# Kernel tuning notes

Hardware: AMD Instinct MI355X
Metric: run time of the kernel (lower is better)

The kernel has to match this reference:

```python
import jax, jax.numpy as jnp
import numpy as np

EMB = 1024
NH = 16
HS = EMB // NH

def setup_inputs() -> dict:
    key = jax.random.key(0)
    ks = jax.random.split(key, 9)
    s = 0.02
    x = jax.random.normal(ks[0], (4, 2048, EMB), dtype=jnp.float32)
    Wq = jax.random.normal(ks[1], (EMB, EMB), dtype=jnp.float32) * s
    bq = jnp.zeros((EMB,), jnp.float32)
    Wk = jax.random.normal(ks[2], (EMB, EMB), dtype=jnp.float32) * s
    bk = jnp.zeros((EMB,), jnp.float32)
    Wv = jax.random.normal(ks[3], (EMB, EMB), dtype=jnp.float32) * s
    bv = jnp.zeros((EMB,), jnp.float32)
    Wo = jax.random.normal(ks[4], (EMB, EMB), dtype=jnp.float32) * s
    bo = jnp.zeros((EMB,), jnp.float32)
    return {"x": x, "Wq": Wq, "bq": bq, "Wk": Wk, "bk": bk,
            "Wv": Wv, "bv": bv, "Wo": Wo, "bo": bo}

def reference(x, Wq, bq, Wk, bk, Wv, bv, Wo, bo):
    B, T, C = x.shape
    q = x @ Wq + bq
    k = x @ Wk + bk
    v = x @ Wv + bv
    # [B, H, T, hs]
    q = q.reshape(B, T, NH, HS).transpose(0, 2, 1, 3)
    k = k.reshape(B, T, NH, HS).transpose(0, 2, 1, 3)
    v = v.reshape(B, T, NH, HS).transpose(0, 2, 1, 3)
    scale = 1.0 / np.sqrt(HS).astype(np.float32)
    att = jnp.einsum('bhqd,bhkd->bhqk', q, k) * scale
    causal = jnp.tril(jnp.ones((T, T), dtype=bool))
    att = jnp.where(causal[None, None], att, jnp.float32(-jnp.inf))
    att = jax.nn.softmax(att, axis=-1)
    y = jnp.einsum('bhqk,bhkd->bhqd', att, v)
    y = y.transpose(0, 2, 1, 3).reshape(B, T, C)
    return y @ Wo + bo
```

## Files before the change

kernel.cpp:

```cpp
#include <hip/hip_runtime.h>

#define EMB   1024
#define NHEAD 16
#define HS    64
#define BATCH 4
#define SEQ   2048
#define MTOK  (BATCH*SEQ)

typedef __bf16 bf16;
typedef __bf16 bf16x8 __attribute__((ext_vector_type(8)));
typedef __bf16 bf16x4 __attribute__((ext_vector_type(4)));
typedef float  f32x4  __attribute__((ext_vector_type(4)));
typedef _Float16 f16;
typedef f16 f16x4 __attribute__((ext_vector_type(4)));
typedef f16 f16x8 __attribute__((ext_vector_type(8)));

#define MFMA16(a,b,c)     __builtin_amdgcn_mfma_f32_16x16x32_bf16(a,b,c,0,0,0)
#define MFMA_H32(a,b,c)   __builtin_amdgcn_mfma_f32_16x16x32_f16(a,b,c,0,0,0)
#define MFMA_H16(a,b,c)   __builtin_amdgcn_mfma_f32_16x16x16f16(a,b,c,0,0,0)

#if __has_builtin(__builtin_amdgcn_exp2f)
#define EXP2(x) __builtin_amdgcn_exp2f(x)
#else
#define EXP2(x) exp2f(x)
#endif

#define GLL(g, l) __builtin_amdgcn_global_load_lds(                         \
        (const __attribute__((address_space(1))) void*)(g),                 \
        (__attribute__((address_space(3))) void*)(l), 16, 0, 0)

__global__ __launch_bounds__(256) void k_prep(
        const float* __restrict__ x, bf16* __restrict__ xb,
        const float* __restrict__ W0, const float* __restrict__ W1,
        const float* __restrict__ W2, const float* __restrict__ W3,
        bf16* __restrict__ T0, bf16* __restrict__ T1,
        bf16* __restrict__ T2, bf16* __restrict__ T3) {
    const int z = blockIdx.z;
    if (z == 0) {
        const int blk = blockIdx.y * 16 + blockIdx.x;
        const size_t base = (size_t)blk * 32768;
        for (int j = threadIdx.x; j < 8192; j += 256) {
            size_t i = base + (size_t)j * 4;
            float4 v = *(const float4*)(x + i);
            bf16x4 o;
            o[0] = (bf16)v.x; o[1] = (bf16)v.y; o[2] = (bf16)v.z; o[3] = (bf16)v.w;
            *(bf16x4*)(xb + i) = o;
        }
        return;
    }
    __shared__ float tile[64][65];
    const float* W = (z == 1) ? W0 : (z == 2) ? W1 : (z == 3) ? W2 : W3;
    bf16* Wt = (z == 1) ? T0 : (z == 2) ? T1 : (z == 3) ? T2 : T3;
    int c0 = blockIdx.x * 64, r0 = blockIdx.y * 64;
    int tx = threadIdx.x & 63, ty = threadIdx.x >> 6;
    #pragma unroll
    for (int r = ty; r < 64; r += 4)
        tile[r][tx] = W[(r0 + r) * EMB + c0 + tx];
    __syncthreads();
    #pragma unroll
    for (int cc = ty; cc < 64; cc += 4)
        Wt[(c0 + cc) * EMB + r0 + tx] = (bf16)tile[tx][cc];
}

__global__ __launch_bounds__(512, 2) void k_qkv_gemm(
        const bf16* __restrict__ xb,
        const bf16* __restrict__ Wqt, const bf16* __restrict__ Wkt, const bf16* __restrict__ Wvt,
        const float* __restrict__ bq, const float* __restrict__ bk, const float* __restrict__ bv,
        f16* __restrict__ Q, f16* __restrict__ K, f16* __restrict__ Vt) {
    __shared__ __align__(16) bf16 As[2][8192];
    __shared__ __align__(16) bf16 Bs[2][8192];
    const int tid = threadIdx.x;
    const int lane = tid & 63;
    const int l15 = lane & 15, quad = lane >> 4;
    const int wave = tid >> 6;
    const int wm = wave >> 2;
    const int wn = wave & 3;

    const int mt = blockIdx.x;
    const int nt = blockIdx.y;
    const int which = nt >> 2;
    const int n0 = (nt & 3) * 256;

    const bf16* Wt   = (which == 0) ? Wqt : (which == 1) ? Wkt : Wvt;
    const float* bias = (which == 0) ? bq : (which == 1) ? bk : bv;

    const bf16* Abase = xb + (size_t)mt * 256 * EMB;
    const bf16* Bbase = Wt + (size_t)n0 * EMB;

    const int P   = tid >> 3, s8 = tid & 7;
    const int cch = s8 ^ (P & 7);
    const int r_  = 2 * P + (cch >> 2);
    const int kc8 = (cch & 3) * 8;
    const bf16* Asrc = Abase + (size_t)r_ * EMB + kc8;
    const bf16* Bsrc = Bbase + (size_t)r_ * EMB + kc8;

#define STAGE_A(T, cb) do {                                                  \
    GLL(Asrc + (T) * 32,             &As[cb][tid * 8]);                      \
    GLL(Asrc + 128 * EMB + (T) * 32, &As[cb][tid * 8 + 4096]); } while (0)
#define STAGE_B(T, cb) do {                                                  \
    GLL(Bsrc + (T) * 32,             &Bs[cb][tid * 8]);                      \
    GLL(Bsrc + 128 * EMB + (T) * 32, &Bs[cb][tid * 8 + 4096]); } while (0)

    int aoff[8], boff[4];
    #pragma unroll
    for (int mf = 0; mf < 8; mf++) {
        const int row = wm * 128 + mf * 16 + l15;
        const int Pr = row >> 1, hh = row & 1;
        aoff[mf] = Pr * 64 + ((((hh << 2) | quad)) ^ (Pr & 7)) * 8;
    }
    #pragma unroll
    for (int nf = 0; nf < 4; nf++) {
        const int row = wn * 64 + nf * 16 + l15;
        const int Pr = row >> 1, hh = row & 1;
        boff[nf] = Pr * 64 + ((((hh << 2) | quad)) ^ (Pr & 7)) * 8;
    }

    f32x4 acc[8][4];
    #pragma unroll
    for (int i = 0; i < 8; i++)
        #pragma unroll
        for (int j = 0; j < 4; j++) acc[i][j] = (f32x4){0.f, 0.f, 0.f, 0.f};

#define BARX __builtin_amdgcn_s_barrier()
#define PRI1 __builtin_amdgcn_s_setprio(1)
#define PRI0 __builtin_amdgcn_s_setprio(0)
#define SCHB __builtin_amdgcn_sched_barrier(0)
#define VM0 asm volatile("s_waitcnt vmcnt(0)" ::: "memory")

    STAGE_A(0, 0); STAGE_B(0, 0);
    SCHB; VM0; BARX;

    bf16x8 a[4], b[4], a2[4];
    #pragma unroll 1
    for (int W = 0; W < 31; ++W) {
        const int c = W & 1;
        const bf16* Ab = As[c];
        const bf16* Bb = Bs[c];
        #pragma unroll
        for (int i = 0; i < 4; i++) a[i] = *(const bf16x8*)(Ab + aoff[i]);
        #pragma unroll
        for (int j = 0; j < 4; j++) b[j] = *(const bf16x8*)(Bb + boff[j]);
        STAGE_A(W + 1, c ^ 1);
        SCHB;
        BARX; PRI1;
        #pragma unroll
        for (int i = 0; i < 4; i++)
            #pragma unroll
            for (int j = 0; j < 4; j++)
                acc[i][j] = MFMA16(a[i], b[j], acc[i][j]);
        PRI0;
        #pragma unroll
        for (int i = 0; i < 4; i++) a2[i] = *(const bf16x8*)(Ab + aoff[4 + i]);
        STAGE_B(W + 1, c ^ 1);
        SCHB; VM0; BARX;
        PRI1;
        #pragma unroll
        for (int i = 0; i < 4; i++)
            #pragma unroll
            for (int j = 0; j < 4; j++)
                acc[4 + i][j] = MFMA16(a2[i], b[j], acc[4 + i][j]);
        PRI0;
    }
    {
        const bf16* Ab = As[1];
        const bf16* Bb = Bs[1];
        #pragma unroll
        for (int i = 0; i < 4; i++) a[i] = *(const bf16x8*)(Ab + aoff[i]);
        #pragma unroll
        for (int j = 0; j < 4; j++) b[j] = *(const bf16x8*)(Bb + boff[j]);
        #pragma unroll
        for (int i = 0; i < 4; i++) a2[i] = *(const bf16x8*)(Ab + aoff[4 + i]);
        #pragma unroll
        for (int i = 0; i < 4; i++)
            #pragma unroll
            for (int j = 0; j < 4; j++) {
                acc[i][j]     = MFMA16(a[i],  b[j], acc[i][j]);
                acc[4 + i][j] = MFMA16(a2[i], b[j], acc[4 + i][j]);
            }
    }
#undef STAGE_A
#undef STAGE_B

    const float QSCALE = 0.18033688011112043f;
    const int h = (n0 >> 6) + wn;
    if (which == 2) {
        #pragma unroll
        for (int nf = 0; nf < 4; nf++) {
            const float bv_ = bias[n0 + wn * 64 + nf * 16 + l15];
            const int d = nf * 16 + l15;
            #pragma unroll
            for (int mf = 0; mf < 8; mf++) {
                const int row0 = mt * 256 + wm * 128 + mf * 16 + quad * 4;
                const int b_ = row0 >> 11, tk0 = row0 & (SEQ - 1);
                f16x4 vv;
                #pragma unroll
                for (int r = 0; r < 4; r++) vv[r] = (f16)(acc[mf][nf][r] + bv_);
                *(f16x4*)(Vt + (((size_t)(b_ * NHEAD + h) * 32 + (tk0 >> 6)) * 64 + d) * 64
                          + (tk0 & 63)) = vv;
            }
        }
    } else {
        f16* OUT = (which == 0) ? Q : K;
        const float scl = (which == 0) ? QSCALE : 1.0f;
        float bvv[4];
        #pragma unroll
        for (int nf = 0; nf < 4; nf++) bvv[nf] = bias[n0 + wn * 64 + nf * 16 + l15];
        #pragma unroll
        for (int mf = 0; mf < 8; mf++) {
            const int row0 = mt * 256 + wm * 128 + mf * 16 + quad * 4;
            const int b_ = row0 >> 11, tk0 = row0 & (SEQ - 1);
            #pragma unroll
            for (int r = 0; r < 4; r++) {
                f16* op = OUT + ((size_t)(b_ * NHEAD + h) * SEQ + (tk0 + r)) * HS + l15;
                #pragma unroll
                for (int nf = 0; nf < 4; nf++)
                    op[nf * 16] = (f16)((acc[mf][nf][r] + bvv[nf]) * scl);
            }
        }
    }
}

__global__ __launch_bounds__(256) void k_attn(
        const f16* __restrict__ Q, const f16* __restrict__ K,
        const f16* __restrict__ Vt, bf16* __restrict__ y) {
    __shared__ __align__(16) f16 kbuf[2][64 * 64];
    __shared__ __align__(16) f16 vbuf[2][64 * 64];
    const int tid = threadIdx.x;
    const int wave = tid >> 6, lane = tid & 63;
    const int l15 = lane & 15, quad = lane >> 4;

    const int L = blockIdx.x;
    const int xcd = L & 7, s = L >> 3;
    const int bh = xcd * 8 + (s & 7);
    const int qt = 15 - (s >> 3);
    const int h = bh & (NHEAD - 1), b_ = bh >> 4;

    const f16* Qb = Q + (size_t)bh * SEQ * HS;
    const f16* Kb = K + (size_t)bh * SEQ * HS;
    const f16* Vb = Vt + (size_t)bh * 32 * 4096;

    const int c0 = tid, c1 = tid + 256;
    const int soff0 = (c0 >> 3) * 64 + (((c0 & 7) ^ ((c0 >> 3) & 7)) * 8);
    const int soff1 = (c1 >> 3) * 64 + (((c1 & 7) ^ ((c1 >> 3) & 7)) * 8);
    const int swz = l15 & 7;

    f16x4 ones;
    #pragma unroll
    for (int i = 0; i < 4; i++) ones[i] = (f16)1.0f;

    const int ntiles = 2 * qt + 2;
    const int qrow0 = qt * 128 + wave * 32;

    f16x8 qb[2][2];
    #pragma unroll
    for (int qf = 0; qf < 2; qf++)
        #pragma unroll
        for (int dk = 0; dk < 2; dk++)
            qb[qf][dk] = *(const f16x8*)(Qb + (qrow0 + 16 * qf + l15) * HS + 32 * dk + quad * 8);

    f32x4 o[2][4], lacc[2];
    #pragma unroll
    for (int qf = 0; qf < 2; qf++) {
        lacc[qf] = (f32x4){0.f, 0.f, 0.f, 0.f};
        #pragma unroll
        for (int df = 0; df < 4; df++) o[qf][df] = (f32x4){0.f, 0.f, 0.f, 0.f};
    }

    f16x8 kr0 = *(const f16x8*)(Kb + c0 * 8);
    f16x8 kr1 = *(const f16x8*)(Kb + c1 * 8);
    f16x8 vr0 = *(const f16x8*)(Vb + c0 * 8);
    f16x8 vr1 = *(const f16x8*)(Vb + c1 * 8);
    *(f16x8*)(kbuf[0] + soff0) = kr0;
    *(f16x8*)(kbuf[0] + soff1) = kr1;
    *(f16x8*)(vbuf[0] + soff0) = vr0;
    *(f16x8*)(vbuf[0] + soff1) = vr1;

    for (int it = 0; it < ntiles; ++it) {
        const int kv0 = it * 64;
        __syncthreads();
        if (it + 1 < ntiles) {
            const f16* kg = Kb + (size_t)(kv0 + 64) * HS;
            const f16* vg = Vb + (size_t)(it + 1) * 4096;
            kr0 = *(const f16x8*)(kg + c0 * 8);
            kr1 = *(const f16x8*)(kg + c1 * 8);
            vr0 = *(const f16x8*)(vg + c0 * 8);
            vr1 = *(const f16x8*)(vg + c1 * 8);
        }
        if (kv0 <= qrow0 + 31) {
            const f16* kb_ = kbuf[it & 1];
            const f16* vb_ = vbuf[it & 1];

            f32x4 sreg[4][2];
            #pragma unroll
            for (int mb = 0; mb < 4; mb++) {
                f16x8 ka0 = *(const f16x8*)(kb_ + (16 * mb + l15) * 64 + ((quad ^ swz) * 8));
                f16x8 ka1 = *(const f16x8*)(kb_ + (16 * mb + l15) * 64 + (((4 + quad) ^ swz) * 8));
                #pragma unroll
                for (int qf = 0; qf < 2; qf++) {
                    f32x4 t = (f32x4){0.f, 0.f, 0.f, 0.f};
                    t = MFMA_H32(ka0, qb[qf][0], t);
                    t = MFMA_H32(ka1, qb[qf][1], t);
                    sreg[mb][qf] = t;
                }
            }

            f16x4 pa[4][2];
            const bool edge = (kv0 + 63 > qrow0);
            #pragma unroll
            for (int mb = 0; mb < 4; mb++)
                #pragma unroll
                for (int qf = 0; qf < 2; qf++) {
                    f16x4 p;
                    if (edge) {
                        #pragma unroll
                        for (int r = 0; r < 4; r++) {
                            const int kvc = kv0 + 16 * mb + quad * 4 + r;
                            const int qq  = qrow0 + 16 * qf + l15;
                            p[r] = (f16)((kvc <= qq) ? EXP2(sreg[mb][qf][r]) : 0.f);
                        }
                    } else {
                        #pragma unroll
                        for (int r = 0; r < 4; r++)
                            p[r] = (f16)EXP2(sreg[mb][qf][r]);
                    }
                    pa[mb][qf] = p;
                }

            #pragma unroll
            for (int df = 0; df < 4; df++)
                #pragma unroll
                for (int kb = 0; kb < 4; kb++) {
                    f16x4 vfrag = *(const f16x4*)(vb_ + (16 * df + l15) * 64 +
                                    (((2 * kb + (quad >> 1)) ^ swz) * 8) + (quad & 1) * 4);
                    #pragma unroll
                    for (int qf = 0; qf < 2; qf++)
                        o[qf][df] = MFMA_H16(pa[kb][qf], vfrag, o[qf][df]);
                }
            #pragma unroll
            for (int kb = 0; kb < 4; kb++)
                #pragma unroll
                for (int qf = 0; qf < 2; qf++)
                    lacc[qf] = MFMA_H16(pa[kb][qf], ones, lacc[qf]);
        }
        if (it + 1 < ntiles) {
            const int nb = (it + 1) & 1;
            *(f16x8*)(kbuf[nb] + soff0) = kr0;
            *(f16x8*)(kbuf[nb] + soff1) = kr1;
            *(f16x8*)(vbuf[nb] + soff0) = vr0;
            *(f16x8*)(vbuf[nb] + soff1) = vr1;
        }
    }

    #pragma unroll
    for (int qf = 0; qf < 2; qf++)
        #pragma unroll
        for (int r = 0; r < 4; r++) {
            float inv = 1.f / lacc[qf][r];
            int t = qrow0 + 16 * qf + quad * 4 + r;
            bf16* yp = y + ((size_t)(b_ * SEQ + t)) * EMB + h * HS;
            #pragma unroll
            for (int df = 0; df < 4; df++)
                yp[df * 16 + l15] = (bf16)(o[qf][df][r] * inv);
        }
}

__global__ __launch_bounds__(256) void k_out_gemm(
        const bf16* __restrict__ y, const bf16* __restrict__ Wot,
        const float* __restrict__ bo, float* __restrict__ out) {
    __shared__ __align__(16) bf16 As[128 * 64];
    __shared__ __align__(16) bf16 Bs[128 * 64];
    const int tid = threadIdx.x;
    const int lane = tid & 63;
    const int wave = tid >> 6;
    const int l15 = lane & 15, quad = lane >> 4;
    const int wm = (wave >> 1) * 64, wn = (wave & 1) * 64;
    const int m0 = blockIdx.x * 128;
    const int n0 = blockIdx.y * 128;

    f32x4 acc[4][4];
    #pragma unroll
    for (int i = 0; i < 4; i++)
        #pragma unroll
        for (int j = 0; j < 4; j++) acc[i][j] = (f32x4){0.f, 0.f, 0.f, 0.f};

    const int r0_ = tid >> 3;
    const int kcs = ((tid & 7) ^ (r0_ & 7)) * 8;
    const bf16* Ag = y   + (size_t)m0 * EMB + r0_ * EMB + kcs;
    const bf16* Bg = Wot + (size_t)n0 * EMB + r0_ * EMB + kcs;
    const int rsw = l15 & 7;

    for (int k0 = 0; k0 < EMB; k0 += 64) {
        __syncthreads();
        #pragma unroll
        for (int g = 0; g < 4; g++) {
            GLL(Ag + 32 * g * EMB + k0, As + (tid + g * 256) * 8);
            GLL(Bg + 32 * g * EMB + k0, Bs + (tid + g * 256) * 8);
        }
        __syncthreads();

        bf16x8 af[2][4], bfr[2][4];
        #pragma unroll
        for (int h = 0; h < 2; h++) {
            #pragma unroll
            for (int rf = 0; rf < 4; rf++)
                af[h][rf] = *(const bf16x8*)(As + (wm + rf * 16 + l15) * 64 +
                                             (((4 * h + quad) ^ rsw) * 8));
            #pragma unroll
            for (int cf = 0; cf < 4; cf++)
                bfr[h][cf] = *(const bf16x8*)(Bs + (wn + cf * 16 + l15) * 64 +
                                              (((4 * h + quad) ^ rsw) * 8));
        }
        #pragma unroll
        for (int h = 0; h < 2; h++)
            #pragma unroll
            for (int rf = 0; rf < 4; rf++)
                #pragma unroll
                for (int cf = 0; cf < 4; cf++)
                    acc[rf][cf] = MFMA16(af[h][rf], bfr[h][cf], acc[rf][cf]);
    }

    #pragma unroll
    for (int cf = 0; cf < 4; cf++) {
        const int col = n0 + wn + cf * 16 + l15;
        const float bv_ = bo[col];
        #pragma unroll
        for (int rf = 0; rf < 4; rf++) {
            #pragma unroll
            for (int r = 0; r < 4; r++) {
                const int row = m0 + wm + rf * 16 + quad * 4 + r;
                out[(size_t)row * EMB + col] = acc[rf][cf][r] + bv_;
            }
        }
    }
}

extern "C" void kernel_launch(void* const* d_in, const int* in_sizes, int n_in,
                              void* d_out, int out_size, void* d_ws, size_t ws_size,
                              hipStream_t stream) {
    const float* x  = (const float*)d_in[0];
    const float* Wq = (const float*)d_in[1];
    const float* bq = (const float*)d_in[2];
    const float* Wk = (const float*)d_in[3];
    const float* bk = (const float*)d_in[4];
    const float* Wv = (const float*)d_in[5];
    const float* bv = (const float*)d_in[6];
    const float* Wo = (const float*)d_in[7];
    const float* bo = (const float*)d_in[8];
    float* out = (float*)d_out;

    char* ws = (char*)d_ws;
    bf16* xb  = (bf16*)(ws);
    bf16* Wqt = (bf16*)(ws + (16u << 20));
    bf16* Wkt = (bf16*)(ws + (18u << 20));
    bf16* Wvt = (bf16*)(ws + (20u << 20));
    bf16* Wot = (bf16*)(ws + (22u << 20));
    f16*  Q   = (f16*)(ws + (24u << 20));
    f16*  K   = (f16*)(ws + (40u << 20));
    f16*  Vt  = (f16*)(ws + (56u << 20));
    bf16* y   = (bf16*)(ws + (72u << 20));

    dim3 gp(16, 16, 5);
    k_prep<<<gp, 256, 0, stream>>>(x, xb, Wq, Wk, Wv, Wo, Wqt, Wkt, Wvt, Wot);

    dim3 g1(32, 12);
    k_qkv_gemm<<<g1, 512, 0, stream>>>(xb, Wqt, Wkt, Wvt, bq, bk, bv, Q, K, Vt);

    dim3 g2(1024);
    k_attn<<<g2, 256, 0, stream>>>(Q, K, Vt, y);

    dim3 g3(MTOK / 128, EMB / 128);
    k_out_gemm<<<g3, 256, 0, stream>>>(y, Wot, bo, out);
}
```

Measured before the change: 271.8 us.

## Retile fused QKV GEMM to 256x192 tiles over concatenated weights

The QKV projection GEMM now treats Wq/Wk/Wv as one contiguous 3072-row transposed weight and uses 256x192 output tiles, giving a 32x16 grid (512 blocks) instead of 32x12 (384 blocks). Each wave computes a 64x96 sub-tile, and the epilogue picks Q, K or V per column fragment. This aims for better occupancy and wave balance across CUs. It depends on Wqt/Wkt/Wvt being laid out contiguously in the workspace, and the B-tile load is now only partially filled by the second half of the threads.

```diff
diff --git a/kernel.cpp b/kernel.cpp
--- a/kernel.cpp
+++ b/kernel.cpp
@@ -64,28 +64,24 @@
 
 __global__ __launch_bounds__(512, 2) void k_qkv_gemm(
         const bf16* __restrict__ xb,
-        const bf16* __restrict__ Wqt, const bf16* __restrict__ Wkt, const bf16* __restrict__ Wvt,
+        const bf16* __restrict__ Wall,
         const float* __restrict__ bq, const float* __restrict__ bk, const float* __restrict__ bv,
         f16* __restrict__ Q, f16* __restrict__ K, f16* __restrict__ Vt) {
     __shared__ __align__(16) bf16 As[2][8192];
-    __shared__ __align__(16) bf16 Bs[2][8192];
+    __shared__ __align__(16) bf16 Bs[2][6144];
     const int tid = threadIdx.x;
     const int lane = tid & 63;
     const int l15 = lane & 15, quad = lane >> 4;
     const int wave = tid >> 6;
-    const int wm = wave >> 2;
-    const int wn = wave & 3;
+    const int wm4 = wave & 3;
+    const int wn2 = wave >> 2;
 
     const int mt = blockIdx.x;
     const int nt = blockIdx.y;
-    const int which = nt >> 2;
-    const int n0 = (nt & 3) * 256;
-
-    const bf16* Wt   = (which == 0) ? Wqt : (which == 1) ? Wkt : Wvt;
-    const float* bias = (which == 0) ? bq : (which == 1) ? bk : bv;
-
-    const bf16* Abase = xb + (size_t)mt * 256 * EMB;
-    const bf16* Bbase = Wt + (size_t)n0 * EMB;
+    const int n0 = nt * 192;
+
+    const bf16* Abase = xb   + (size_t)mt * 256 * EMB;
+    const bf16* Bbase = Wall + (size_t)n0 * EMB;
 
     const int P   = tid >> 3, s8 = tid & 7;
     const int cch = s8 ^ (P & 7);
@@ -99,27 +95,29 @@
     GLL(Asrc + 128 * EMB + (T) * 32, &As[cb][tid * 8 + 4096]); } while (0)
 #define STAGE_B(T, cb) do {                                                  \
     GLL(Bsrc + (T) * 32,             &Bs[cb][tid * 8]);                      \
-    GLL(Bsrc + 128 * EMB + (T) * 32, &Bs[cb][tid * 8 + 4096]); } while (0)
-
-    int aoff[8], boff[4];
-    #pragma unroll
-    for (int mf = 0; mf < 8; mf++) {
-        const int row = wm * 128 + mf * 16 + l15;
+    if (tid < 256)                                                           \
+        GLL(Bsrc + 128 * EMB + (T) * 32, &Bs[cb][tid * 8 + 4096]);           \
+} while (0)
+
+    int aoff[4], boff[6];
+    #pragma unroll
+    for (int mf = 0; mf < 4; mf++) {
+        const int row = wm4 * 64 + mf * 16 + l15;
         const int Pr = row >> 1, hh = row & 1;
         aoff[mf] = Pr * 64 + ((((hh << 2) | quad)) ^ (Pr & 7)) * 8;
     }
     #pragma unroll
-    for (int nf = 0; nf < 4; nf++) {
-        const int row = wn * 64 + nf * 16 + l15;
+    for (int nf = 0; nf < 6; nf++) {
+        const int row = wn2 * 96 + nf * 16 + l15;
         const int Pr = row >> 1, hh = row & 1;
         boff[nf] = Pr * 64 + ((((hh << 2) | quad)) ^ (Pr & 7)) * 8;
     }
 
-    f32x4 acc[8][4];
-    #pragma unroll
-    for (int i = 0; i < 8; i++)
-        #pragma unroll
-        for (int j = 0; j < 4; j++) acc[i][j] = (f32x4){0.f, 0.f, 0.f, 0.f};
+    f32x4 acc[4][6];
+    #pragma unroll
+    for (int i = 0; i < 4; i++)
+        #pragma unroll
+        for (int j = 0; j < 6; j++) acc[i][j] = (f32x4){0.f, 0.f, 0.f, 0.f};
 
 #define BARX __builtin_amdgcn_s_barrier()
 #define PRI1 __builtin_amdgcn_s_setprio(1)
@@ -130,7 +128,7 @@
     STAGE_A(0, 0); STAGE_B(0, 0);
     SCHB; VM0; BARX;
 
-    bf16x8 a[4], b[4], a2[4];
+    bf16x8 a[4], b[3], b2[3];
     #pragma unroll 1
     for (int W = 0; W < 31; ++W) {
         const int c = W & 1;
@@ -139,26 +137,26 @@
         #pragma unroll
         for (int i = 0; i < 4; i++) a[i] = *(const bf16x8*)(Ab + aoff[i]);
         #pragma unroll
-        for (int j = 0; j < 4; j++) b[j] = *(const bf16x8*)(Bb + boff[j]);
+        for (int j = 0; j < 3; j++) b[j] = *(const bf16x8*)(Bb + boff[j]);
         STAGE_A(W + 1, c ^ 1);
         SCHB;
         BARX; PRI1;
         #pragma unroll
         for (int i = 0; i < 4; i++)
             #pragma unroll
-            for (int j = 0; j < 4; j++)
+            for (int j = 0; j < 3; j++)
                 acc[i][j] = MFMA16(a[i], b[j], acc[i][j]);
         PRI0;
         #pragma unroll
-        for (int i = 0; i < 4; i++) a2[i] = *(const bf16x8*)(Ab + aoff[4 + i]);
+        for (int j = 0; j < 3; j++) b2[j] = *(const bf16x8*)(Bb + boff[3 + j]);
         STAGE_B(W + 1, c ^ 1);
         SCHB; VM0; BARX;
         PRI1;
         #pragma unroll
         for (int i = 0; i < 4; i++)
             #pragma unroll
-            for (int j = 0; j < 4; j++)
-                acc[4 + i][j] = MFMA16(a2[i], b[j], acc[4 + i][j]);
+            for (int j = 0; j < 3; j++)
+                acc[i][3 + j] = MFMA16(a[i], b2[j], acc[i][3 + j]);
         PRI0;
     }
     {
@@ -167,30 +165,32 @@
         #pragma unroll
         for (int i = 0; i < 4; i++) a[i] = *(const bf16x8*)(Ab + aoff[i]);
         #pragma unroll
-        for (int j = 0; j < 4; j++) b[j] = *(const bf16x8*)(Bb + boff[j]);
-        #pragma unroll
-        for (int i = 0; i < 4; i++) a2[i] = *(const bf16x8*)(Ab + aoff[4 + i]);
+        for (int j = 0; j < 3; j++) b[j]  = *(const bf16x8*)(Bb + boff[j]);
+        #pragma unroll
+        for (int j = 0; j < 3; j++) b2[j] = *(const bf16x8*)(Bb + boff[3 + j]);
         #pragma unroll
         for (int i = 0; i < 4; i++)
             #pragma unroll
-            for (int j = 0; j < 4; j++) {
-                acc[i][j]     = MFMA16(a[i],  b[j], acc[i][j]);
-                acc[4 + i][j] = MFMA16(a2[i], b[j], acc[4 + i][j]);
+            for (int j = 0; j < 3; j++) {
+                acc[i][j]     = MFMA16(a[i], b[j],  acc[i][j]);
+                acc[i][3 + j] = MFMA16(a[i], b2[j], acc[i][3 + j]);
             }
     }
 #undef STAGE_A
 #undef STAGE_B
 
     const float QSCALE = 0.18033688011112043f;
-    const int h = (n0 >> 6) + wn;
-    if (which == 2) {
-        #pragma unroll
-        for (int nf = 0; nf < 4; nf++) {
-            const float bv_ = bias[n0 + wn * 64 + nf * 16 + l15];
-            const int d = nf * 16 + l15;
-            #pragma unroll
-            for (int mf = 0; mf < 8; mf++) {
-                const int row0 = mt * 256 + wm * 128 + mf * 16 + quad * 4;
+    #pragma unroll
+    for (int nf = 0; nf < 6; nf++) {
+        const int col = n0 + wn2 * 96 + nf * 16 + l15;
+        const int whichf = col >> 10;
+        const int cc = col & 1023;
+        const int h = cc >> 6, d = cc & 63;
+        const float bv_ = (whichf == 0) ? bq[cc] : (whichf == 1) ? bk[cc] : bv[cc];
+        if (whichf == 2) {
+            #pragma unroll
+            for (int mf = 0; mf < 4; mf++) {
+                const int row0 = mt * 256 + wm4 * 64 + mf * 16 + quad * 4;
                 const int b_ = row0 >> 11, tk0 = row0 & (SEQ - 1);
                 f16x4 vv;
                 #pragma unroll
@@ -198,23 +198,17 @@
                 *(f16x4*)(Vt + (((size_t)(b_ * NHEAD + h) * 32 + (tk0 >> 6)) * 64 + d) * 64
                           + (tk0 & 63)) = vv;
             }
-        }
-    } else {
-        f16* OUT = (which == 0) ? Q : K;
-        const float scl = (which == 0) ? QSCALE : 1.0f;
-        float bvv[4];
-        #pragma unroll
-        for (int nf = 0; nf < 4; nf++) bvv[nf] = bias[n0 + wn * 64 + nf * 16 + l15];
-        #pragma unroll
-        for (int mf = 0; mf < 8; mf++) {
-            const int row0 = mt * 256 + wm * 128 + mf * 16 + quad * 4;
-            const int b_ = row0 >> 11, tk0 = row0 & (SEQ - 1);
-            #pragma unroll
-            for (int r = 0; r < 4; r++) {
-                f16* op = OUT + ((size_t)(b_ * NHEAD + h) * SEQ + (tk0 + r)) * HS + l15;
-                #pragma unroll
-                for (int nf = 0; nf < 4; nf++)
-                    op[nf * 16] = (f16)((acc[mf][nf][r] + bvv[nf]) * scl);
+        } else {
+            f16* OUT = (whichf == 0) ? Q : K;
+            const float scl = (whichf == 0) ? QSCALE : 1.0f;
+            #pragma unroll
+            for (int mf = 0; mf < 4; mf++) {
+                const int row0 = mt * 256 + wm4 * 64 + mf * 16 + quad * 4;
+                const int b_ = row0 >> 11, tk0 = row0 & (SEQ - 1);
+                #pragma unroll
+                for (int r = 0; r < 4; r++)
+                    OUT[((size_t)(b_ * NHEAD + h) * SEQ + (tk0 + r)) * HS + d] =
+                        (f16)((acc[mf][nf][r] + bv_) * scl);
             }
         }
     }
@@ -462,8 +456,8 @@
     dim3 gp(16, 16, 5);
     k_prep<<<gp, 256, 0, stream>>>(x, xb, Wq, Wk, Wv, Wo, Wqt, Wkt, Wvt, Wot);
 
-    dim3 g1(32, 12);
-    k_qkv_gemm<<<g1, 512, 0, stream>>>(xb, Wqt, Wkt, Wvt, bq, bk, bv, Q, K, Vt);
+    dim3 g1(32, 16);
+    k_qkv_gemm<<<g1, 512, 0, stream>>>(xb, Wqt, bq, bk, bv, Q, K, Vt);
 
     dim3 g2(1024);
     k_attn<<<g2, 256, 0, stream>>>(Q, K, Vt, y);
```

After: 264.9 us (median of 2 runs). 1.03x faster.
